# Kernel optimization log

Hardware: AMD Instinct MI355X
Metric: run time of the kernel (lower is better)

The kernel has to match this reference:

```python
import jax, jax.numpy as jnp
import numpy as np

N_NODES = 100000
N_EDGES = 1600000
N_GRAPHS = 64
EPS = 1e-16  # matches PyG softmax eps


def _glorot(key, shape):
    fan_in, fan_out = shape[0], shape[1]
    lim = np.sqrt(6.0 / (fan_in + fan_out))
    return jax.random.uniform(key, shape, jnp.float32, -lim, lim)


def setup_inputs() -> dict:
    key = jax.random.key(0)
    ks = jax.random.split(key, 20)
    x = jax.random.normal(ks[0], (N_NODES, 3), jnp.float32)
    edge_index = jax.random.randint(ks[1], (2, N_EDGES), 0, N_NODES, jnp.int64)
    batch = jnp.sort(jax.random.randint(ks[2], (N_NODES,), 0, N_GRAPHS, jnp.int64))
    p = {
        # gat1: TransformerConv(3 -> 32, heads=2, concat) => H*D = 64
        'Wq1': _glorot(ks[3], (3, 64)),  'bq1': jnp.zeros((64,), jnp.float32),
        'Wk1': _glorot(ks[4], (3, 64)),  'bk1': jnp.zeros((64,), jnp.float32),
        'Wv1': _glorot(ks[5], (3, 64)),  'bv1': jnp.zeros((64,), jnp.float32),
        'Ws1': _glorot(ks[6], (3, 64)),  'bs1': jnp.zeros((64,), jnp.float32),
        # gat2: TransformerConv(64 -> 64, heads=2, concat) => H*D = 128
        'Wq2': _glorot(ks[7], (64, 128)), 'bq2': jnp.zeros((128,), jnp.float32),
        'Wk2': _glorot(ks[8], (64, 128)), 'bk2': jnp.zeros((128,), jnp.float32),
        'Wv2': _glorot(ks[9], (64, 128)), 'bv2': jnp.zeros((128,), jnp.float32),
        'Ws2': _glorot(ks[10], (64, 128)), 'bs2': jnp.zeros((128,), jnp.float32),
        # MLP head
        'W1': _glorot(ks[11], (128, 32)),  'b1': jnp.zeros((32,), jnp.float32),
        'W2': _glorot(ks[12], (32, 128)),  'b2': jnp.zeros((128,), jnp.float32),
        'W3': _glorot(ks[13], (128, 40)),  'b3': jnp.zeros((40,), jnp.float32),
    }
    return {'x': x, 'edge_index': edge_index, 'batch': batch, **p}


def transformer_conv(x, src, dst, Wq, bq, Wk, bk, Wv, bv, Ws, bs, heads, d):
    """PyG TransformerConv (concat=True, root_weight=True, no edge_attr, no beta)."""
    n = x.shape[0]
    q = (x @ Wq + bq).reshape(n, heads, d)
    k = (x @ Wk + bk).reshape(n, heads, d)
    v = (x @ Wv + bv).reshape(n, heads, d)
    # gather per edge: query at target (i = dst), key/value at source (j = src)
    logits = jnp.einsum('ehd,ehd->eh', q[dst], k[src]) / jnp.sqrt(jnp.float32(d))  # [E,H]
    # segment softmax over incoming edges of each target node
    m = jax.ops.segment_max(logits, dst, num_segments=n)          # [N,H]
    m = jnp.where(jnp.isfinite(m), m, 0.0)
    e = jnp.exp(logits - m[dst])                                   # [E,H]
    s = jax.ops.segment_sum(e, dst, num_segments=n)                # [N,H]
    alpha = e / (s[dst] + EPS)                                     # [E,H]
    out = jax.ops.segment_sum(alpha[:, :, None] * v[src], dst, num_segments=n)  # [N,H,D]
    out = out.reshape(n, heads * d)
    return out + (x @ Ws + bs)  # skip connection (root_weight)


def global_max_pool(x, batch, num_graphs):
    return jax.ops.segment_max(x, batch, num_segments=num_graphs)


def reference(x, edge_index, batch,
              Wq1, bq1, Wk1, bk1, Wv1, bv1, Ws1, bs1,
              Wq2, bq2, Wk2, bk2, Wv2, bv2, Ws2, bs2,
              W1, b1, W2, b2, W3, b3):
    src, dst = edge_index[0], edge_index[1]
    h = jax.nn.relu(transformer_conv(x, src, dst, Wq1, bq1, Wk1, bk1, Wv1, bv1, Ws1, bs1, heads=2, d=32))
    h = jax.nn.relu(transformer_conv(h, src, dst, Wq2, bq2, Wk2, bk2, Wv2, bv2, Ws2, bs2, heads=2, d=64))
    g = global_max_pool(h, batch, N_GRAPHS)            # [G,128]
    latent = jax.nn.relu(g @ W1 + b1)                   # [G,32]
    h2 = jax.nn.relu(latent @ W2 + b2)                  # [G,128]
    logits = h2 @ W3 + b3                               # [G,40]
    return (logits, latent)
```

## Files before the change

kernel.cpp:

```cpp
#include <hip/hip_runtime.h>
#include <hip/hip_bf16.h>

typedef __hip_bfloat16 bf16;
typedef unsigned short u16;
typedef unsigned int u32;
typedef __attribute__((ext_vector_type(8))) short bf16x8;
typedef __attribute__((ext_vector_type(4))) float f32x4;
typedef __attribute__((ext_vector_type(2))) float f32x2;

#define NN 100000
#define NE 1600000
#define NG 64
#define NBKT 196
#define EPB 4096
#define NBLK ((NE + EPB - 1) / EPB)

__device__ __forceinline__ float ldf(const void* __restrict__ p, int i, int isbf) {
    return isbf ? __bfloat162float(((const bf16*)p)[i]) : ((const float*)p)[i];
}

__device__ __forceinline__ int ld_idx(const int* __restrict__ p, int i, int is64) {
    return is64 ? p[2 * i] : p[i];
}

__device__ __forceinline__ u16 f2bu(float f) {
    u32 u = __float_as_uint(f);
    u32 r = u + 0x7fffu + ((u >> 16) & 1u);
    return (u16)(r >> 16);
}
__device__ __forceinline__ float blo(u32 u) { return __uint_as_float(u << 16); }
__device__ __forceinline__ float bhi(u32 u) { return __uint_as_float(u & 0xffff0000u); }

__global__ void k_detect(const int* __restrict__ ei, const int* __restrict__ bat,
                         const u16* __restrict__ xw, int* __restrict__ flags) {
    __shared__ int anyE, anyB, cntF;
    if (threadIdx.x == 0) { anyE = 0; anyB = 0; cntF = 0; }
    __syncthreads();
    int t = threadIdx.x;
    int accE = 0, accB = 0;
#pragma unroll
    for (int i = 0; i < 8; i++) {
        int si = t * 8 + i;
        long long pe = ((long long)si * (2LL * NE)) / 2048;
        int ie = ((int)pe) | 1;
        if (ie < 2 * NE) accE |= ei[ie];
    }
    {
        int ib = (int)(((long long)t * NN) / 256) | 1;
        if (ib < NN) accB |= bat[ib];
    }
    if (accE) atomicOr(&anyE, 1);
    if (accB) atomicOr(&anyB, 1);
    {
        u16 w = xw[2 * t];
        int hb = (w >> 8) & 0x7F;
        if (hb >= 0x3B && hb <= 0x41) atomicAdd(&cntF, 1);
    }
    __syncthreads();
    if (threadIdx.x == 0) {
        flags[0] = anyE ? 0 : 1;
        flags[1] = anyB ? 0 : 1;
        flags[2] = (cntF > 128) ? 1 : 0;
    }
}

__global__ void k_p1hist(const int* __restrict__ ei, const int* __restrict__ flags,
                         int* __restrict__ bhistT) {
    __shared__ int lh[NBKT];
    int t = threadIdx.x;
    if (t < NBKT) lh[t] = 0;
    __syncthreads();
    int is64 = flags[0];
    int base = blockIdx.x * EPB;
#pragma unroll
    for (int i = 0; i < EPB / 512; i++) {
        int e = base + i * 512 + t;
        if (e < NE) {
            int di = ld_idx(ei, NE + e, is64);
            atomicAdd(&lh[di >> 9], 1);
        }
    }
    __syncthreads();
    if (t < NBKT) bhistT[t * NBLK + blockIdx.x] = lh[t];
}

__global__ void k_p2a(const int* __restrict__ bhistT, int* __restrict__ boffT,
                      int* __restrict__ btot) {
    __shared__ int sh[512];
    int b = blockIdx.x, t = threadIdx.x;
    int v = (t < NBLK) ? bhistT[b * NBLK + t] : 0;
    sh[t] = v;
    __syncthreads();
#pragma unroll
    for (int off = 1; off < 512; off <<= 1) {
        int y = (t >= off) ? sh[t - off] : 0;
        __syncthreads();
        sh[t] += y;
        __syncthreads();
    }
    if (t < NBLK) boffT[b * NBLK + t] = sh[t] - v;
    if (t == 511) btot[b] = sh[511];
}

__global__ void k_p2b(const int* __restrict__ btot, int* __restrict__ bbase) {
    __shared__ int sh[256];
    int t = threadIdx.x;
    int v = (t < NBKT) ? btot[t] : 0;
    sh[t] = v;
    __syncthreads();
#pragma unroll
    for (int off = 1; off < 256; off <<= 1) {
        int y = (t >= off) ? sh[t - off] : 0;
        __syncthreads();
        sh[t] += y;
        __syncthreads();
    }
    if (t < NBKT) bbase[t] = sh[t] - v;
    if (t == 255) bbase[NBKT] = sh[255];
}

__global__ void k_p3part(const int* __restrict__ ei, const int* __restrict__ flags,
                         const int* __restrict__ boffT, const int* __restrict__ bbase,
                         int2* __restrict__ pairs) {
    __shared__ int loff[NBKT];
    int t = threadIdx.x;
    if (t < NBKT) loff[t] = bbase[t] + boffT[t * NBLK + blockIdx.x];
    __syncthreads();
    int is64 = flags[0];
    int base = blockIdx.x * EPB;
#pragma unroll
    for (int i = 0; i < EPB / 512; i++) {
        int e = base + i * 512 + t;
        if (e < NE) {
            int sj = ld_idx(ei, e, is64);
            int di = ld_idx(ei, NE + e, is64);
            int pos = atomicAdd(&loff[di >> 9], 1);
            pairs[pos] = {di, sj};
        }
    }
}

__global__ void k_p4sort(const int2* __restrict__ pairs, const int* __restrict__ bbase,
                         int* __restrict__ rowptr, int* __restrict__ es) {
    __shared__ int lcnt[512], pfx[512];
    int b = blockIdx.x, t = threadIdx.x;
    int bb = bbase[b];
    int bend = bbase[b + 1];
    int n0 = b << 9;
    lcnt[t] = 0;
    __syncthreads();
    for (int p = bb + t; p < bend; p += 512)
        atomicAdd(&lcnt[pairs[p].x - n0], 1);
    __syncthreads();
    int v = lcnt[t];
    pfx[t] = v;
    __syncthreads();
#pragma unroll
    for (int off = 1; off < 512; off <<= 1) {
        int y = (t >= off) ? pfx[t - off] : 0;
        __syncthreads();
        pfx[t] += y;
        __syncthreads();
    }
    int start = bb + pfx[t] - v;
    int n = n0 + t;
    if (n < NN) rowptr[n] = start;
    lcnt[t] = start;
    if (b == NBKT - 1 && t == 0) rowptr[NN] = NE;
    __syncthreads();
    for (int p = bb + t; p < bend; p += 512) {
        int2 pr = pairs[p];
        int pos = atomicAdd(&lcnt[pr.x - n0], 1);
        es[pos] = pr.y;
    }
}

__global__ void k_qkvs1(const void* __restrict__ x,
                        const void* __restrict__ Wq, const void* __restrict__ bq,
                        const void* __restrict__ Wk, const void* __restrict__ bk,
                        const void* __restrict__ Wv, const void* __restrict__ bv,
                        const void* __restrict__ Ws, const void* __restrict__ bs,
                        const int* __restrict__ flags,
                        u16* __restrict__ q1b, u16* __restrict__ kv1,
                        u16* __restrict__ s1b) {
    int idx = blockIdx.x * blockDim.x + threadIdx.x;
    if (idx >= NN * 64) return;
    int fb = flags[2];
    int n = idx >> 6, d = idx & 63;
    float x0 = ldf(x, n * 3 + 0, fb);
    float x1 = ldf(x, n * 3 + 1, fb);
    float x2 = ldf(x, n * 3 + 2, fb);
    q1b[idx] = f2bu(x0 * ldf(Wq, d, fb) + x1 * ldf(Wq, 64 + d, fb) + x2 * ldf(Wq, 128 + d, fb) + ldf(bq, d, fb));
    kv1[(size_t)n * 128 + d] =
        f2bu(x0 * ldf(Wk, d, fb) + x1 * ldf(Wk, 64 + d, fb) + x2 * ldf(Wk, 128 + d, fb) + ldf(bk, d, fb));
    kv1[(size_t)n * 128 + 64 + d] =
        f2bu(x0 * ldf(Wv, d, fb) + x1 * ldf(Wv, 64 + d, fb) + x2 * ldf(Wv, 128 + d, fb) + ldf(bv, d, fb));
    s1b[idx] = f2bu(x0 * ldf(Ws, d, fb) + x1 * ldf(Ws, 64 + d, fb) + x2 * ldf(Ws, 128 + d, fb) + ldf(bs, d, fb));
}

__global__ void k_attn1(const int* __restrict__ rowptr, const int* __restrict__ es,
                        const u16* __restrict__ q1b, const u16* __restrict__ kv1,
                        const u16* __restrict__ s1b, u16* __restrict__ h1b) {
    int w = (blockIdx.x * blockDim.x + threadIdx.x) >> 6;
    if (w >= NN) return;
    int lane = threadIdx.x & 63;
    int g = lane >> 4, hl = lane & 15;
    const float scale = 0.17677669529663687f;
    uint2 qu = ((const uint2*)(q1b + (size_t)w * 64))[hl];
    float qs0 = blo(qu.x) * scale, qs1 = bhi(qu.x) * scale;
    float qs2 = blo(qu.y) * scale, qs3 = bhi(qu.y) * scale;
    float l = 0.0f, o0 = 0.0f, o1 = 0.0f, o2 = 0.0f, o3 = 0.0f;
    int beg = rowptr[w], end = rowptr[w + 1];
    int iters = (end - beg + 3) >> 2;
#define PROC1(ku, vu, vld) { \
    float t = qs0 * blo(ku.x) + qs1 * bhi(ku.x) + qs2 * blo(ku.y) + qs3 * bhi(ku.y); \
    t += __shfl_xor(t, 4, 64); t += __shfl_xor(t, 2, 64); t += __shfl_xor(t, 1, 64); \
    float e = (vld) ? __expf(t) : 0.0f; \
    l += e; \
    o0 += e * blo(vu.x); o1 += e * bhi(vu.x); \
    o2 += e * blo(vu.y); o3 += e * bhi(vu.y); }
    if (iters > 0) {
        int pA = beg + g;
        int vA = pA < end; int sjA = es[vA ? pA : beg];
        uint2 kA = ((const uint2*)(kv1 + (size_t)sjA * 128))[hl];
        uint2 uA = ((const uint2*)(kv1 + (size_t)sjA * 128 + 64))[hl];
        int pB = pA + 4;
        int vB = pB < end; int sjB = es[vB ? pB : beg];
        uint2 kB = ((const uint2*)(kv1 + (size_t)sjB * 128))[hl];
        uint2 uB = ((const uint2*)(kv1 + (size_t)sjB * 128 + 64))[hl];
        int pC = pA + 8;
        int vC = pC < end; int sjC = es[vC ? pC : beg];
        uint2 kC = ((const uint2*)(kv1 + (size_t)sjC * 128))[hl];
        uint2 uC = ((const uint2*)(kv1 + (size_t)sjC * 128 + 64))[hl];
        for (int i = 0; i < iters; i += 3) {
            int pD = pA + 12;
            int vD = pD < end; int sjD = es[vD ? pD : beg];
            uint2 kD = ((const uint2*)(kv1 + (size_t)sjD * 128))[hl];
            uint2 uD = ((const uint2*)(kv1 + (size_t)sjD * 128 + 64))[hl];
            PROC1(kA, uA, vA);
            int pE = pA + 16;
            int vE = pE < end; int sjE = es[vE ? pE : beg];
            uint2 kE = ((const uint2*)(kv1 + (size_t)sjE * 128))[hl];
            uint2 uE = ((const uint2*)(kv1 + (size_t)sjE * 128 + 64))[hl];
            PROC1(kB, uB, vB);
            int pF = pA + 20;
            int vF = pF < end; int sjF = es[vF ? pF : beg];
            uint2 kF = ((const uint2*)(kv1 + (size_t)sjF * 128))[hl];
            uint2 uF = ((const uint2*)(kv1 + (size_t)sjF * 128 + 64))[hl];
            PROC1(kC, uC, vC);
            pA = pD; vA = vD; kA = kD; uA = uD;
            pB = pE; vB = vE; kB = kE; uB = uE;
            pC = pF; vC = vF; kC = kF; uC = uF;
        }
    }
#undef PROC1
#pragma unroll
    for (int off = 16; off <= 32; off <<= 1) {
        l += __shfl_xor(l, off, 64);
        o0 += __shfl_xor(o0, off, 64);
        o1 += __shfl_xor(o1, off, 64);
        o2 += __shfl_xor(o2, off, 64);
        o3 += __shfl_xor(o3, off, 64);
    }
    if (g == 0) {
        float inv = 1.0f / (l + 1e-16f);
        uint2 su = ((const uint2*)(s1b + (size_t)w * 64))[hl];
        uint2 r;
        r.x = (u32)f2bu(fmaxf(blo(su.x) + o0 * inv, 0.0f)) | ((u32)f2bu(fmaxf(bhi(su.x) + o1 * inv, 0.0f)) << 16);
        r.y = (u32)f2bu(fmaxf(blo(su.y) + o2 * inv, 0.0f)) | ((u32)f2bu(fmaxf(bhi(su.y) + o3 * inv, 0.0f)) << 16);
        ((uint2*)(h1b + (size_t)w * 64))[hl] = r;
    }
}

__global__ void k_wprep(const void* __restrict__ Wq, const void* __restrict__ bq,
                        const void* __restrict__ Wk, const void* __restrict__ bk,
                        const void* __restrict__ Wv, const void* __restrict__ bv,
                        const void* __restrict__ Ws, const void* __restrict__ bs,
                        const int* __restrict__ flags,
                        u16* __restrict__ Wt, float* __restrict__ bias,
                        float* __restrict__ g) {
    int idx = blockIdx.x * blockDim.x + threadIdx.x;
    if (idx >= 512 * 64) return;
    if (idx < NG * 128) g[idx] = 0.0f;
    int fb = flags[2];
    int n = idx >> 6, k = idx & 63;
    int mat = n >> 7, c = n & 127;
    const void* W = (mat == 0) ? Wq : (mat == 1) ? Wk : (mat == 2) ? Wv : Ws;
    Wt[n * 64 + k] = f2bu(ldf(W, k * 128 + c, fb));
    if (k == 0) {
        const void* B = (mat == 0) ? bq : (mat == 1) ? bk : (mat == 2) ? bv : bs;
        bias[n] = ldf(B, c, fb);
    }
}

__global__ void k_gemm2(const u16* __restrict__ h1b, const u16* __restrict__ Wt,
                        const float* __restrict__ bias,
                        u16* __restrict__ q2b, u16* __restrict__ kvm,
                        u16* __restrict__ s2b) {
    int w = (blockIdx.x * blockDim.x + threadIdx.x) >> 6;
    if (w >= NN / 16) return;
    int lane = threadIdx.x & 63;
    int quad = lane >> 4, mr = lane & 15;
    int m0 = w * 16;
    const u16* arow = h1b + (size_t)(m0 + mr) * 64 + quad * 8;
    bf16x8 a0 = *(const bf16x8*)(arow);
    bf16x8 a1 = *(const bf16x8*)(arow + 32);
#pragma unroll 4
    for (int n0 = 0; n0 < 512; n0 += 16) {
        const u16* brow = Wt + (size_t)(n0 + mr) * 64 + quad * 8;
        bf16x8 b0 = *(const bf16x8*)(brow);
        bf16x8 b1 = *(const bf16x8*)(brow + 32);
        f32x4 acc = {0.f, 0.f, 0.f, 0.f};
        acc = __builtin_amdgcn_mfma_f32_16x16x32_bf16(a0, b0, acc, 0, 0, 0);
        acc = __builtin_amdgcn_mfma_f32_16x16x32_bf16(a1, b1, acc, 0, 0, 0);
        float bs = bias[n0 + mr];
        int mat = n0 >> 7;
        int c = (n0 & 127) + mr;
#pragma unroll
        for (int r = 0; r < 4; r++) {
            int row = m0 + quad * 4 + r;
            float val = acc[r] + bs;
            if (mat == 1) {
                float nb = __shfl_xor(val, 1, 64);
                if (!(mr & 1)) {
                    int packed = __builtin_amdgcn_cvt_pk_fp8_f32(val, nb, 0, false);
                    *(u16*)((char*)kvm + (size_t)row * 384 + c) = (u16)packed;
                }
            } else if (mat == 0) {
                q2b[(size_t)row * 128 + c] = f2bu(val);
            } else if (mat == 2) {
                kvm[(size_t)row * 192 + 64 + c] = f2bu(val);
            } else {
                s2b[(size_t)row * 128 + c] = f2bu(val);
            }
        }
    }
}

__global__ void k_attn2(const int* __restrict__ rowptr, const int* __restrict__ es,
                        const u16* __restrict__ q2b, const u16* __restrict__ kvm,
                        const u16* __restrict__ s2b, u16* __restrict__ h2b) {
    int w = (blockIdx.x * blockDim.x + threadIdx.x) >> 6;
    if (w >= NN) return;
    int lane = threadIdx.x & 63;
    int g = lane >> 4, hl = lane & 15;
    const float scale = 0.125f;
    uint4 qu = ((const uint4*)(q2b + (size_t)w * 128))[hl];
    float qs[8];
    qs[0] = blo(qu.x) * scale; qs[1] = bhi(qu.x) * scale;
    qs[2] = blo(qu.y) * scale; qs[3] = bhi(qu.y) * scale;
    qs[4] = blo(qu.z) * scale; qs[5] = bhi(qu.z) * scale;
    qs[6] = blo(qu.w) * scale; qs[7] = bhi(qu.w) * scale;
    float l = 0.0f;
    float o[8] = {0.f, 0.f, 0.f, 0.f, 0.f, 0.f, 0.f, 0.f};
    int beg = rowptr[w], end = rowptr[w + 1];
    int iters = (end - beg + 3) >> 2;
#define PROC2(ku, vu, vld) { \
    f32x2 k01 = __builtin_amdgcn_cvt_pk_f32_fp8((int)ku.x, false); \
    f32x2 k23 = __builtin_amdgcn_cvt_pk_f32_fp8((int)ku.x, true); \
    f32x2 k45 = __builtin_amdgcn_cvt_pk_f32_fp8((int)ku.y, false); \
    f32x2 k67 = __builtin_amdgcn_cvt_pk_f32_fp8((int)ku.y, true); \
    float t = qs[0] * k01.x + qs[1] * k01.y + qs[2] * k23.x + qs[3] * k23.y \
            + qs[4] * k45.x + qs[5] * k45.y + qs[6] * k67.x + qs[7] * k67.y; \
    t += __shfl_xor(t, 4, 64); t += __shfl_xor(t, 2, 64); t += __shfl_xor(t, 1, 64); \
    float e = (vld) ? __expf(t) : 0.0f; \
    l += e; \
    o[0] += e * blo(vu.x); o[1] += e * bhi(vu.x); \
    o[2] += e * blo(vu.y); o[3] += e * bhi(vu.y); \
    o[4] += e * blo(vu.z); o[5] += e * bhi(vu.z); \
    o[6] += e * blo(vu.w); o[7] += e * bhi(vu.w); }
    if (iters > 0) {
        int pA = beg + g;
        int vA = pA < end; int sjA = es[vA ? pA : beg];
        uint2 kA = ((const uint2*)(kvm + (size_t)sjA * 192))[hl];
        uint4 uA = ((const uint4*)(kvm + (size_t)sjA * 192 + 64))[hl];
        int pB = pA + 4;
        int vB = pB < end; int sjB = es[vB ? pB : beg];
        uint2 kB = ((const uint2*)(kvm + (size_t)sjB * 192))[hl];
        uint4 uB = ((const uint4*)(kvm + (size_t)sjB * 192 + 64))[hl];
        int pC = pA + 8;
        int vC = pC < end; int sjC = es[vC ? pC : beg];
        uint2 kC = ((const uint2*)(kvm + (size_t)sjC * 192))[hl];
        uint4 uC = ((const uint4*)(kvm + (size_t)sjC * 192 + 64))[hl];
        for (int i = 0; i < iters; i += 3) {
            int pD = pA + 12;
            int vD = pD < end; int sjD = es[vD ? pD : beg];
            uint2 kD = ((const uint2*)(kvm + (size_t)sjD * 192))[hl];
            uint4 uD = ((const uint4*)(kvm + (size_t)sjD * 192 + 64))[hl];
            PROC2(kA, uA, vA);
            int pE = pA + 16;
            int vE = pE < end; int sjE = es[vE ? pE : beg];
            uint2 kE = ((const uint2*)(kvm + (size_t)sjE * 192))[hl];
            uint4 uE = ((const uint4*)(kvm + (size_t)sjE * 192 + 64))[hl];
            PROC2(kB, uB, vB);
            int pF = pA + 20;
            int vF = pF < end; int sjF = es[vF ? pF : beg];
            uint2 kF = ((const uint2*)(kvm + (size_t)sjF * 192))[hl];
            uint4 uF = ((const uint4*)(kvm + (size_t)sjF * 192 + 64))[hl];
            PROC2(kC, uC, vC);
            pA = pD; vA = vD; kA = kD; uA = uD;
            pB = pE; vB = vE; kB = kE; uB = uE;
            pC = pF; vC = vF; kC = kF; uC = uF;
        }
    }
#undef PROC2
#pragma unroll
    for (int off = 16; off <= 32; off <<= 1) {
        l += __shfl_xor(l, off, 64);
#pragma unroll
        for (int j = 0; j < 8; j++) o[j] += __shfl_xor(o[j], off, 64);
    }
    if (g == 0) {
        float inv = 1.0f / (l + 1e-16f);
        uint4 su = ((const uint4*)(s2b + (size_t)w * 128))[hl];
        uint4 r;
        r.x = (u32)f2bu(blo(su.x) + o[0] * inv) | ((u32)f2bu(bhi(su.x) + o[1] * inv) << 16);
        r.y = (u32)f2bu(blo(su.y) + o[2] * inv) | ((u32)f2bu(bhi(su.y) + o[3] * inv) << 16);
        r.z = (u32)f2bu(blo(su.z) + o[4] * inv) | ((u32)f2bu(bhi(su.z) + o[5] * inv) << 16);
        r.w = (u32)f2bu(blo(su.w) + o[6] * inv) | ((u32)f2bu(bhi(su.w) + o[7] * inv) << 16);
        ((uint4*)(h2b + (size_t)w * 128))[hl] = r;
    }
}

__global__ void k_pool(const u16* __restrict__ h2b, const int* __restrict__ batch,
                       const int* __restrict__ flags, float* __restrict__ g) {
    int idx = blockIdx.x * blockDim.x + threadIdx.x;
    if (idx >= (NN / 16) * 128) return;
    int is64 = flags[1];
    int d = idx & 127, ch = idx >> 7;
    int n0 = ch * 16;
    int curb = ld_idx(batch, n0, is64);
    float mx = 0.0f;
    for (int i = 0; i < 16; i++) {
        int n = n0 + i;
        int b = ld_idx(batch, n, is64);
        if (b != curb) {
            atomicMax((int*)&g[curb * 128 + d], __float_as_int(mx));
            mx = 0.0f;
            curb = b;
        }
        mx = fmaxf(mx, __uint_as_float(((u32)h2b[(size_t)n * 128 + d]) << 16));
    }
    atomicMax((int*)&g[curb * 128 + d], __float_as_int(mx));
}

__global__ void k_mlp(const float* __restrict__ g,
                      const void* __restrict__ W1, const void* __restrict__ b1,
                      const void* __restrict__ W2, const void* __restrict__ b2,
                      const void* __restrict__ W3, const void* __restrict__ b3,
                      const int* __restrict__ flags, float* __restrict__ out) {
    __shared__ float gr[128], lat[32], h2[128];
    int gid = blockIdx.x, t = threadIdx.x;
    int fb = flags[2];
    gr[t] = g[gid * 128 + t];
    __syncthreads();
    if (t < 32) {
        float a = ldf(b1, t, fb);
        for (int k = 0; k < 128; k++) a += gr[k] * ldf(W1, k * 32 + t, fb);
        a = fmaxf(a, 0.0f);
        lat[t] = a;
        out[NG * 40 + gid * 32 + t] = a;
    }
    __syncthreads();
    {
        float a = ldf(b2, t, fb);
        for (int k = 0; k < 32; k++) a += lat[k] * ldf(W2, k * 128 + t, fb);
        h2[t] = fmaxf(a, 0.0f);
    }
    __syncthreads();
    if (t < 40) {
        float a = ldf(b3, t, fb);
        for (int k = 0; k < 128; k++) a += h2[k] * ldf(W3, k * 40 + t, fb);
        out[gid * 40 + t] = a;
    }
}

extern "C" void kernel_launch(void* const* d_in, const int* in_sizes, int n_in,
                              void* d_out, int out_size, void* d_ws, size_t ws_size,
                              hipStream_t stream) {
    const void* x     = d_in[0];
    const int*  ei    = (const int*)d_in[1];
    const int*  batch = (const int*)d_in[2];
    const void *Wq1 = d_in[3],  *bq1 = d_in[4];
    const void *Wk1 = d_in[5],  *bk1 = d_in[6];
    const void *Wv1 = d_in[7],  *bv1 = d_in[8];
    const void *Ws1 = d_in[9],  *bs1 = d_in[10];
    const void *Wq2 = d_in[11], *bq2 = d_in[12];
    const void *Wk2 = d_in[13], *bk2 = d_in[14];
    const void *Wv2 = d_in[15], *bv2 = d_in[16];
    const void *Ws2 = d_in[17], *bs2 = d_in[18];
    const void *W1  = d_in[19], *b1  = d_in[20];
    const void *W2  = d_in[21], *b2  = d_in[22];
    const void *W3  = d_in[23], *b3  = d_in[24];

    float* ws = (float*)d_ws;
    float* g    = ws;
    float* bias = g + NG * 128;
    u16* u16base = (u16*)(bias + 512);
    u16* kvm  = u16base;
    u16* kv1  = kvm + (size_t)NN * 192;
    u16* h1b  = kv1 + (size_t)NN * 128;
    u16* q1b  = h1b + (size_t)NN * 64;
    u16* s1b  = q1b + (size_t)NN * 64;
    u16* q2b  = s1b + (size_t)NN * 64;
    u16* s2b  = q2b + (size_t)NN * 128;
    u16* h2b  = s2b + (size_t)NN * 128;
    u16* Wt   = h2b + (size_t)NN * 128;
    int* flags  = (int*)(Wt + 512 * 64);
    int* rowptr = flags + 8;
    int* bhistT = rowptr + NN + 1;
    int* boffT  = bhistT + NBKT * NBLK;
    int* btot   = boffT + NBKT * NBLK;
    int* bbase  = btot + NBKT;
    int* es     = bbase + NBKT + 1;
    int2* pairs = (int2*)kvm;

    float* out  = (float*)d_out;

    const int B = 256;
    k_detect<<<1, 256, 0, stream>>>(ei, batch, (const u16*)x, flags);
    k_p1hist<<<NBLK, 512, 0, stream>>>(ei, flags, bhistT);
    k_p2a<<<NBKT, 512, 0, stream>>>(bhistT, boffT, btot);
    k_p2b<<<1, 256, 0, stream>>>(btot, bbase);
    k_p3part<<<NBLK, 512, 0, stream>>>(ei, flags, boffT, bbase, pairs);
    k_p4sort<<<NBKT, 512, 0, stream>>>(pairs, bbase, rowptr, es);
    k_qkvs1<<<(NN * 64 + B - 1) / B, B, 0, stream>>>(x, Wq1, bq1, Wk1, bk1, Wv1, bv1, Ws1, bs1,
                                                     flags, q1b, kv1, s1b);
    k_attn1<<<(NN * 64 + B - 1) / B, B, 0, stream>>>(rowptr, es, q1b, kv1, s1b, h1b);
    k_wprep<<<(512 * 64 + B - 1) / B, B, 0, stream>>>(Wq2, bq2, Wk2, bk2, Wv2, bv2, Ws2, bs2,
                                                      flags, Wt, bias, g);
    k_gemm2<<<(NN / 16 * 64 + B - 1) / B, B, 0, stream>>>(h1b, Wt, bias, q2b, kvm, s2b);
    k_attn2<<<(NN * 64 + B - 1) / B, B, 0, stream>>>(rowptr, es, q2b, kvm, s2b, h2b);
    k_pool<<<((NN / 16) * 128 + B - 1) / B, B, 0, stream>>>(h2b, batch, flags, g);
    k_mlp<<<NG, 128, 0, stream>>>(g, W1, b1, W2, b2, W3, b3, flags, out);
}
```

Measured before the change: 450.0 us.

## Pack sort pairs to 32-bit, store layer-1 keys as fp8, fuse q/skip into attn1

The partition pass now packs each (dst-local, src) pair into one 32-bit word instead of an int2, which halves the traffic through the sort scratch buffer. Layer-1 keys are quantized to fp8 and stored next to bf16 values in a 96-element row, shrinking the per-edge gather from 256 to 192 bytes. The query and skip projections are recomputed inside the attention kernel from the 3-wide input, so the q1b/s1b buffers are no longer written and read. FP8 keys lower logit precision and could affect accuracy, and the packing assumes source indices fit in 23 bits.

```diff
diff --git a/kernel.cpp b/kernel.cpp
--- a/kernel.cpp
+++ b/kernel.cpp
@@ -121,7 +121,7 @@
 
 __global__ void k_p3part(const int* __restrict__ ei, const int* __restrict__ flags,
                          const int* __restrict__ boffT, const int* __restrict__ bbase,
-                         int2* __restrict__ pairs) {
+                         u32* __restrict__ pairs) {
     __shared__ int loff[NBKT];
     int t = threadIdx.x;
     if (t < NBKT) loff[t] = bbase[t] + boffT[t * NBLK + blockIdx.x];
@@ -135,12 +135,12 @@
             int sj = ld_idx(ei, e, is64);
             int di = ld_idx(ei, NE + e, is64);
             int pos = atomicAdd(&loff[di >> 9], 1);
-            pairs[pos] = {di, sj};
+            pairs[pos] = ((u32)sj << 9) | (u32)(di & 511);
         }
     }
 }
 
-__global__ void k_p4sort(const int2* __restrict__ pairs, const int* __restrict__ bbase,
+__global__ void k_p4sort(const u32* __restrict__ pairs, const int* __restrict__ bbase,
                          int* __restrict__ rowptr, int* __restrict__ es) {
     __shared__ int lcnt[512], pfx[512];
     int b = blockIdx.x, t = threadIdx.x;
@@ -150,7 +150,7 @@
     lcnt[t] = 0;
     __syncthreads();
     for (int p = bb + t; p < bend; p += 512)
-        atomicAdd(&lcnt[pairs[p].x - n0], 1);
+        atomicAdd(&lcnt[pairs[p] & 511u], 1);
     __syncthreads();
     int v = lcnt[t];
     pfx[t] = v;
@@ -169,20 +169,16 @@
     if (b == NBKT - 1 && t == 0) rowptr[NN] = NE;
     __syncthreads();
     for (int p = bb + t; p < bend; p += 512) {
-        int2 pr = pairs[p];
-        int pos = atomicAdd(&lcnt[pr.x - n0], 1);
-        es[pos] = pr.y;
-    }
-}
-
-__global__ void k_qkvs1(const void* __restrict__ x,
-                        const void* __restrict__ Wq, const void* __restrict__ bq,
-                        const void* __restrict__ Wk, const void* __restrict__ bk,
-                        const void* __restrict__ Wv, const void* __restrict__ bv,
-                        const void* __restrict__ Ws, const void* __restrict__ bs,
-                        const int* __restrict__ flags,
-                        u16* __restrict__ q1b, u16* __restrict__ kv1,
-                        u16* __restrict__ s1b) {
+        u32 pr = pairs[p];
+        int pos = atomicAdd(&lcnt[pr & 511u], 1);
+        es[pos] = (int)(pr >> 9);
+    }
+}
+
+__global__ void k_kv1(const void* __restrict__ x,
+                      const void* __restrict__ Wk, const void* __restrict__ bk,
+                      const void* __restrict__ Wv, const void* __restrict__ bv,
+                      const int* __restrict__ flags, u16* __restrict__ kv1m) {
     int idx = blockIdx.x * blockDim.x + threadIdx.x;
     if (idx >= NN * 64) return;
     int fb = flags[2];
@@ -190,30 +186,43 @@
     float x0 = ldf(x, n * 3 + 0, fb);
     float x1 = ldf(x, n * 3 + 1, fb);
     float x2 = ldf(x, n * 3 + 2, fb);
-    q1b[idx] = f2bu(x0 * ldf(Wq, d, fb) + x1 * ldf(Wq, 64 + d, fb) + x2 * ldf(Wq, 128 + d, fb) + ldf(bq, d, fb));
-    kv1[(size_t)n * 128 + d] =
-        f2bu(x0 * ldf(Wk, d, fb) + x1 * ldf(Wk, 64 + d, fb) + x2 * ldf(Wk, 128 + d, fb) + ldf(bk, d, fb));
-    kv1[(size_t)n * 128 + 64 + d] =
-        f2bu(x0 * ldf(Wv, d, fb) + x1 * ldf(Wv, 64 + d, fb) + x2 * ldf(Wv, 128 + d, fb) + ldf(bv, d, fb));
-    s1b[idx] = f2bu(x0 * ldf(Ws, d, fb) + x1 * ldf(Ws, 64 + d, fb) + x2 * ldf(Ws, 128 + d, fb) + ldf(bs, d, fb));
+    float kf = x0 * ldf(Wk, d, fb) + x1 * ldf(Wk, 64 + d, fb) + x2 * ldf(Wk, 128 + d, fb) + ldf(bk, d, fb);
+    float vf = x0 * ldf(Wv, d, fb) + x1 * ldf(Wv, 64 + d, fb) + x2 * ldf(Wv, 128 + d, fb) + ldf(bv, d, fb);
+    float knb = __shfl_xor(kf, 1, 64);
+    if (!(d & 1)) {
+        int packed = __builtin_amdgcn_cvt_pk_fp8_f32(kf, knb, 0, false);
+        kv1m[(size_t)n * 96 + (d >> 1)] = (u16)packed;
+    }
+    kv1m[(size_t)n * 96 + 32 + d] = f2bu(vf);
 }
 
 __global__ void k_attn1(const int* __restrict__ rowptr, const int* __restrict__ es,
-                        const u16* __restrict__ q1b, const u16* __restrict__ kv1,
-                        const u16* __restrict__ s1b, u16* __restrict__ h1b) {
+                        const void* __restrict__ x,
+                        const void* __restrict__ Wq, const void* __restrict__ bq,
+                        const void* __restrict__ Ws, const void* __restrict__ bs,
+                        const int* __restrict__ flags,
+                        const u16* __restrict__ kv1m, u16* __restrict__ h1b) {
     int w = (blockIdx.x * blockDim.x + threadIdx.x) >> 6;
     if (w >= NN) return;
     int lane = threadIdx.x & 63;
     int g = lane >> 4, hl = lane & 15;
+    int fb = flags[2];
+    float x0 = ldf(x, w * 3 + 0, fb);
+    float x1 = ldf(x, w * 3 + 1, fb);
+    float x2 = ldf(x, w * 3 + 2, fb);
     const float scale = 0.17677669529663687f;
-    uint2 qu = ((const uint2*)(q1b + (size_t)w * 64))[hl];
-    float qs0 = blo(qu.x) * scale, qs1 = bhi(qu.x) * scale;
-    float qs2 = blo(qu.y) * scale, qs3 = bhi(qu.y) * scale;
+    int d0 = 4 * hl;
+    float qs0 = (x0 * ldf(Wq, d0 + 0, fb) + x1 * ldf(Wq, 64 + d0 + 0, fb) + x2 * ldf(Wq, 128 + d0 + 0, fb) + ldf(bq, d0 + 0, fb)) * scale;
+    float qs1 = (x0 * ldf(Wq, d0 + 1, fb) + x1 * ldf(Wq, 64 + d0 + 1, fb) + x2 * ldf(Wq, 128 + d0 + 1, fb) + ldf(bq, d0 + 1, fb)) * scale;
+    float qs2 = (x0 * ldf(Wq, d0 + 2, fb) + x1 * ldf(Wq, 64 + d0 + 2, fb) + x2 * ldf(Wq, 128 + d0 + 2, fb) + ldf(bq, d0 + 2, fb)) * scale;
+    float qs3 = (x0 * ldf(Wq, d0 + 3, fb) + x1 * ldf(Wq, 64 + d0 + 3, fb) + x2 * ldf(Wq, 128 + d0 + 3, fb) + ldf(bq, d0 + 3, fb)) * scale;
     float l = 0.0f, o0 = 0.0f, o1 = 0.0f, o2 = 0.0f, o3 = 0.0f;
     int beg = rowptr[w], end = rowptr[w + 1];
     int iters = (end - beg + 3) >> 2;
 #define PROC1(ku, vu, vld) { \
-    float t = qs0 * blo(ku.x) + qs1 * bhi(ku.x) + qs2 * blo(ku.y) + qs3 * bhi(ku.y); \
+    f32x2 k01 = __builtin_amdgcn_cvt_pk_f32_fp8((int)ku, false); \
+    f32x2 k23 = __builtin_amdgcn_cvt_pk_f32_fp8((int)ku, true); \
+    float t = qs0 * k01.x + qs1 * k01.y + qs2 * k23.x + qs3 * k23.y; \
     t += __shfl_xor(t, 4, 64); t += __shfl_xor(t, 2, 64); t += __shfl_xor(t, 1, 64); \
     float e = (vld) ? __expf(t) : 0.0f; \
     l += e; \
@@ -222,31 +231,31 @@
     if (iters > 0) {
         int pA = beg + g;
         int vA = pA < end; int sjA = es[vA ? pA : beg];
-        uint2 kA = ((const uint2*)(kv1 + (size_t)sjA * 128))[hl];
-        uint2 uA = ((const uint2*)(kv1 + (size_t)sjA * 128 + 64))[hl];
+        u32 kA = *(const u32*)(kv1m + (size_t)sjA * 96 + hl * 2);
+        uint2 uA = *(const uint2*)(kv1m + (size_t)sjA * 96 + 32 + hl * 4);
         int pB = pA + 4;
         int vB = pB < end; int sjB = es[vB ? pB : beg];
-        uint2 kB = ((const uint2*)(kv1 + (size_t)sjB * 128))[hl];
-        uint2 uB = ((const uint2*)(kv1 + (size_t)sjB * 128 + 64))[hl];
+        u32 kB = *(const u32*)(kv1m + (size_t)sjB * 96 + hl * 2);
+        uint2 uB = *(const uint2*)(kv1m + (size_t)sjB * 96 + 32 + hl * 4);
         int pC = pA + 8;
         int vC = pC < end; int sjC = es[vC ? pC : beg];
-        uint2 kC = ((const uint2*)(kv1 + (size_t)sjC * 128))[hl];
-        uint2 uC = ((const uint2*)(kv1 + (size_t)sjC * 128 + 64))[hl];
+        u32 kC = *(const u32*)(kv1m + (size_t)sjC * 96 + hl * 2);
+        uint2 uC = *(const uint2*)(kv1m + (size_t)sjC * 96 + 32 + hl * 4);
         for (int i = 0; i < iters; i += 3) {
             int pD = pA + 12;
             int vD = pD < end; int sjD = es[vD ? pD : beg];
-            uint2 kD = ((const uint2*)(kv1 + (size_t)sjD * 128))[hl];
-            uint2 uD = ((const uint2*)(kv1 + (size_t)sjD * 128 + 64))[hl];
+            u32 kD = *(const u32*)(kv1m + (size_t)sjD * 96 + hl * 2);
+            uint2 uD = *(const uint2*)(kv1m + (size_t)sjD * 96 + 32 + hl * 4);
             PROC1(kA, uA, vA);
             int pE = pA + 16;
             int vE = pE < end; int sjE = es[vE ? pE : beg];
-            uint2 kE = ((const uint2*)(kv1 + (size_t)sjE * 128))[hl];
-            uint2 uE = ((const uint2*)(kv1 + (size_t)sjE * 128 + 64))[hl];
+            u32 kE = *(const u32*)(kv1m + (size_t)sjE * 96 + hl * 2);
+            uint2 uE = *(const uint2*)(kv1m + (size_t)sjE * 96 + 32 + hl * 4);
             PROC1(kB, uB, vB);
             int pF = pA + 20;
             int vF = pF < end; int sjF = es[vF ? pF : beg];
-            uint2 kF = ((const uint2*)(kv1 + (size_t)sjF * 128))[hl];
-            uint2 uF = ((const uint2*)(kv1 + (size_t)sjF * 128 + 64))[hl];
+            u32 kF = *(const u32*)(kv1m + (size_t)sjF * 96 + hl * 2);
+            uint2 uF = *(const uint2*)(kv1m + (size_t)sjF * 96 + 32 + hl * 4);
             PROC1(kC, uC, vC);
             pA = pD; vA = vD; kA = kD; uA = uD;
             pB = pE; vB = vE; kB = kE; uB = uE;
@@ -264,10 +273,13 @@
     }
     if (g == 0) {
         float inv = 1.0f / (l + 1e-16f);
-        uint2 su = ((const uint2*)(s1b + (size_t)w * 64))[hl];
+        float sv0 = x0 * ldf(Ws, d0 + 0, fb) + x1 * ldf(Ws, 64 + d0 + 0, fb) + x2 * ldf(Ws, 128 + d0 + 0, fb) + ldf(bs, d0 + 0, fb);
+        float sv1 = x0 * ldf(Ws, d0 + 1, fb) + x1 * ldf(Ws, 64 + d0 + 1, fb) + x2 * ldf(Ws, 128 + d0 + 1, fb) + ldf(bs, d0 + 1, fb);
+        float sv2 = x0 * ldf(Ws, d0 + 2, fb) + x1 * ldf(Ws, 64 + d0 + 2, fb) + x2 * ldf(Ws, 128 + d0 + 2, fb) + ldf(bs, d0 + 2, fb);
+        float sv3 = x0 * ldf(Ws, d0 + 3, fb) + x1 * ldf(Ws, 64 + d0 + 3, fb) + x2 * ldf(Ws, 128 + d0 + 3, fb) + ldf(bs, d0 + 3, fb);
         uint2 r;
-        r.x = (u32)f2bu(fmaxf(blo(su.x) + o0 * inv, 0.0f)) | ((u32)f2bu(fmaxf(bhi(su.x) + o1 * inv, 0.0f)) << 16);
-        r.y = (u32)f2bu(fmaxf(blo(su.y) + o2 * inv, 0.0f)) | ((u32)f2bu(fmaxf(bhi(su.y) + o3 * inv, 0.0f)) << 16);
+        r.x = (u32)f2bu(fmaxf(sv0 + o0 * inv, 0.0f)) | ((u32)f2bu(fmaxf(sv1 + o1 * inv, 0.0f)) << 16);
+        r.y = (u32)f2bu(fmaxf(sv2 + o2 * inv, 0.0f)) | ((u32)f2bu(fmaxf(sv3 + o3 * inv, 0.0f)) << 16);
         ((uint2*)(h1b + (size_t)w * 64))[hl] = r;
     }
 }
@@ -497,15 +509,13 @@
     float* g    = ws;
     float* bias = g + NG * 128;
     u16* u16base = (u16*)(bias + 512);
-    u16* kvm  = u16base;
-    u16* kv1  = kvm + (size_t)NN * 192;
-    u16* h1b  = kv1 + (size_t)NN * 128;
-    u16* q1b  = h1b + (size_t)NN * 64;
-    u16* s1b  = q1b + (size_t)NN * 64;
-    u16* q2b  = s1b + (size_t)NN * 64;
-    u16* s2b  = q2b + (size_t)NN * 128;
-    u16* h2b  = s2b + (size_t)NN * 128;
-    u16* Wt   = h2b + (size_t)NN * 128;
+    u16* kvm   = u16base;
+    u16* kv1m  = kvm + (size_t)NN * 192;
+    u16* h1b   = kv1m + (size_t)NN * 96;
+    u16* q2b   = h1b + (size_t)NN * 64;
+    u16* s2b   = q2b + (size_t)NN * 128;
+    u16* h2b   = s2b + (size_t)NN * 128;
+    u16* Wt    = h2b + (size_t)NN * 128;
     int* flags  = (int*)(Wt + 512 * 64);
     int* rowptr = flags + 8;
     int* bhistT = rowptr + NN + 1;
@@ -513,7 +523,7 @@
     int* btot   = boffT + NBKT * NBLK;
     int* bbase  = btot + NBKT;
     int* es     = bbase + NBKT + 1;
-    int2* pairs = (int2*)kvm;
+    u32* pairs = (u32*)kvm;
 
     float* out  = (float*)d_out;
 
@@ -524,9 +534,9 @@
     k_p2b<<<1, 256, 0, stream>>>(btot, bbase);
     k_p3part<<<NBLK, 512, 0, stream>>>(ei, flags, boffT, bbase, pairs);
     k_p4sort<<<NBKT, 512, 0, stream>>>(pairs, bbase, rowptr, es);
-    k_qkvs1<<<(NN * 64 + B - 1) / B, B, 0, stream>>>(x, Wq1, bq1, Wk1, bk1, Wv1, bv1, Ws1, bs1,
-                                                     flags, q1b, kv1, s1b);
-    k_attn1<<<(NN * 64 + B - 1) / B, B, 0, stream>>>(rowptr, es, q1b, kv1, s1b, h1b);
+    k_kv1<<<(NN * 64 + B - 1) / B, B, 0, stream>>>(x, Wk1, bk1, Wv1, bv1, flags, kv1m);
+    k_attn1<<<(NN * 64 + B - 1) / B, B, 0, stream>>>(rowptr, es, x, Wq1, bq1, Ws1, bs1,
+                                                     flags, kv1m, h1b);
     k_wprep<<<(512 * 64 + B - 1) / B, B, 0, stream>>>(Wq2, bq2, Wk2, bk2, Wv2, bv2, Ws2, bs2,
                                                       flags, Wt, bias, g);
     k_gemm2<<<(NN / 16 * 64 + B - 1) / B, B, 0, stream>>>(h1b, Wt, bias, q2b, kvm, s2b);
```

Result: slower. 506.9 us (+12.6%).
